# Kernel tuning notes

Measured on AMD Instinct MI355X. Metric: run time of the kernel, lower is better.

Reference implementation:

```python
import jax, jax.numpy as jnp
import numpy as np

B, N, D, H, F, K, L, V, E, C = 8, 256, 768, 8, 3072, 128, 8, 32, 1024, 2
HD = D // H
LN_EPS = 1e-3  # keras LayerNormalization default epsilon
GAUSS_A = (2.0 * 3.14159) ** 0.5  # constant from source


def _ln(x, g, b):
    m = jnp.mean(x, axis=-1, keepdims=True)
    v = jnp.mean((x - m) ** 2, axis=-1, keepdims=True)
    return (x - m) * jax.lax.rsqrt(v + LN_EPS) * g + b


def _gelu(x):
    return jax.nn.gelu(x, approximate=False)  # keras 'gelu' is exact


def setup_inputs() -> dict:
    key = jax.random.key(0)
    ks = iter(jax.random.split(key, 40))
    s = 0.02
    inp = {
        'dist': jax.random.uniform(next(ks), (B, N, N), jnp.float32) * 10.0,
        'tok_emb': jax.random.normal(next(ks), (V, D), jnp.float32) * s,
        'gmeans': jax.random.uniform(next(ks), (K,), jnp.float32) * 3.0,
        'gstds': jax.random.uniform(next(ks), (K,), jnp.float32) * 3.0,
        'gmul': jnp.ones((E, 1), jnp.float32),
        'gbias': jnp.zeros((E, 1), jnp.float32),
        'gp1w': jax.random.normal(next(ks), (K, K), jnp.float32) * s,
        'gp1b': jnp.zeros((K,), jnp.float32),
        'gp2w': jax.random.normal(next(ks), (K, H), jnp.float32) * s,
        'gp2b': jnp.zeros((H,), jnp.float32),
        'emb_ln_g': jnp.ones((D,), jnp.float32),
        'emb_ln_b': jnp.zeros((D,), jnp.float32),
        'Wq': jax.random.normal(next(ks), (L, D, D), jnp.float32) * s,
        'bq': jnp.zeros((L, D), jnp.float32),
        'Wo': jax.random.normal(next(ks), (L, D, D), jnp.float32) * s,
        'bo': jnp.zeros((L, D), jnp.float32),
        'ln1g': jnp.ones((L, D), jnp.float32),
        'ln1b': jnp.zeros((L, D), jnp.float32),
        'W1': jax.random.normal(next(ks), (L, D, F), jnp.float32) * s,
        'b1': jnp.zeros((L, F), jnp.float32),
        'W2': jax.random.normal(next(ks), (L, F, D), jnp.float32) * s,
        'b2': jnp.zeros((L, D), jnp.float32),
        'ln2g': jnp.ones((L, D), jnp.float32),
        'ln2b': jnp.zeros((L, D), jnp.float32),
        'fin_ln_g': jnp.ones((D,), jnp.float32),
        'fin_ln_b': jnp.zeros((D,), jnp.float32),
        'cls_w1': jax.random.normal(next(ks), (D, D), jnp.float32) * s,
        'cls_b1': jnp.zeros((D,), jnp.float32),
        'cls_w2': jax.random.normal(next(ks), (D, C), jnp.float32) * s,
        'cls_b2': jnp.zeros((C,), jnp.float32),
        'tokens': jax.random.randint(next(ks), (B, N), 0, V, jnp.int64),
        'edge_type': jax.random.randint(next(ks), (B, N, N), 0, E, jnp.int64),
    }
    return inp


def _forward(dist, tok_emb, gmeans, gstds, gmul, gbias, gp1w, gp1b, gp2w, gp2b,
             emb_ln_g, emb_ln_b, Wq, bq, Wo, bo, ln1g, ln1b, W1, b1, W2, b2,
             ln2g, ln2b, fin_ln_g, fin_ln_b, cls_w1, cls_b1, cls_w2, cls_b2,
             tokens, edge_type):
    # --- Gaussian pairwise bias ---
    mul = gmul[edge_type][..., 0]      # (B,N,N)
    add = gbias[edge_type][..., 0]     # (B,N,N)
    y = mul * dist + add               # (B,N,N)
    std = jnp.abs(gstds) + 1e-5        # (K,)
    g = jnp.exp(-0.5 * ((y[..., None] - gmeans) / std) ** 2) / (GAUSS_A * std)  # (B,N,N,K)
    pb = _gelu(g @ gp1w + gp1b) @ gp2w + gp2b   # (B,N,N,H)
    attn_bias = jnp.transpose(pb, (0, 3, 1, 2))  # (B,H,N,N)

    # --- encoder (pre-LN), NB: wq is shared for q/k/v as in source ---
    x = tok_emb[tokens]                # (B,N,D)
    x = _ln(x, emb_ln_g, emb_ln_b)
    scale = 1.0 / np.sqrt(HD).astype(np.float32)

    def split_heads(t):
        return t.reshape(B, N, H, HD).transpose(0, 2, 1, 3)  # (B,H,N,HD)

    for i in range(L):
        r = x
        h = _ln(x, ln1g[i], ln1b[i])
        q = split_heads((h @ Wq[i] + bq[i]) * scale)
        k = split_heads(h @ Wq[i] + bq[i])
        v = split_heads(h @ Wq[i] + bq[i])
        s = jnp.einsum('bhnd,bhmd->bhnm', q, k) + attn_bias
        p = jax.nn.softmax(s, axis=-1)
        o = jnp.einsum('bhnm,bhmd->bhnd', p, v)
        o = o.transpose(0, 2, 1, 3).reshape(B, N, D) @ Wo[i] + bo[i]
        x = o + r
        r = x
        h = _ln(x, ln2g[i], ln2b[i])
        x = _gelu(h @ W1[i] + b1[i]) @ W2[i] + b2[i] + r
    x = _ln(x, fin_ln_g, fin_ln_b)

    # --- classification head on CLS token ---
    cls = x[:, 0, :]
    return _gelu(cls @ cls_w1 + cls_b1) @ cls_w2 + cls_b2  # (B,C)


def reference(dist, tok_emb, gmeans, gstds, gmul, gbias, gp1w, gp1b, gp2w, gp2b,
              emb_ln_g, emb_ln_b, Wq, bq, Wo, bo, ln1g, ln1b, W1, b1, W2, b2,
              ln2g, ln2b, fin_ln_g, fin_ln_b, cls_w1, cls_b1, cls_w2, cls_b2,
              tokens, edge_type):
    return _forward(dist, tok_emb, gmeans, gstds, gmul, gbias, gp1w, gp1b, gp2w,
                    gp2b, emb_ln_g, emb_ln_b, Wq, bq, Wo, bo, ln1g, ln1b, W1, b1,
                    W2, b2, ln2g, ln2b, fin_ln_g, fin_ln_b, cls_w1, cls_b1,
                    cls_w2, cls_b2, tokens, edge_type)
```

## Files before the change

### kernel.cpp

```cpp
#include <hip/hip_runtime.h>
#include <hip/hip_bf16.h>
#include <math.h>


#define DEV_INLINE __device__ __forceinline__

typedef __attribute__((ext_vector_type(8))) short short8v;
typedef __attribute__((ext_vector_type(4))) short short4v;
typedef __attribute__((ext_vector_type(4))) float f32x4;

typedef __attribute__((address_space(1))) const unsigned int GLD_SRC;
typedef __attribute__((address_space(3))) unsigned int LDS_DST;

DEV_INLINE void gload16(const unsigned short* g, unsigned short* l) {
  __builtin_amdgcn_global_load_lds((GLD_SRC*)(const void*)g, (LDS_DST*)(void*)l, 16, 0, 0);
}
DEV_INLINE unsigned short f2bf(float f) {
  unsigned u = __float_as_uint(f);
  return (unsigned short)((u + 0x7fffu + ((u >> 16) & 1u)) >> 16);
}
DEV_INLINE unsigned short f2bf_hw(float f) {
  __hip_bfloat16 h = __float2bfloat16(f);
  unsigned short u; __builtin_memcpy(&u, &h, 2); return u;
}
DEV_INLINE float gelu_f(float v) {
  return 0.5f * v * (1.0f + erff(v * 0.70710678118654752f));
}
DEV_INLINE float gelu_tanh(float x) {
  float x2 = x * x;
  float t  = x * fmaf(0.044715f, x2, 1.0f);
  float e  = __builtin_amdgcn_exp2f(2.3022082f * t);
  return x * e * __frcp_rn(e + 1.0f);
}
DEV_INLINE f32x4 zero4() { f32x4 z; z[0]=0.f; z[1]=0.f; z[2]=0.f; z[3]=0.f; return z; }

__global__ __launch_bounds__(256) void k_cast_t(
    const float* __restrict__ W, unsigned short* __restrict__ Wt, int K, int N)
{
  __shared__ float s[64][68];
  const int tid = threadIdx.x;
  const size_t lay = (size_t)blockIdx.z * K * N;
  const int k0 = blockIdx.x * 64, n0 = blockIdx.y * 64;
  const int r = tid >> 4, c4 = (tid & 15) << 2;
  #pragma unroll
  for (int i = 0; i < 4; ++i)
    *(float4*)&s[r + i * 16][c4] =
        *(const float4*)(W + lay + (size_t)(k0 + r + i * 16) * N + n0 + c4);
  __syncthreads();
  const int n = tid & 63, kc = (tid >> 6) << 4;
  short8v v0, v1;
  #pragma unroll
  for (int j = 0; j < 8; ++j) v0[j] = (short)f2bf(s[kc + j][n]);
  #pragma unroll
  for (int j = 0; j < 8; ++j) v1[j] = (short)f2bf(s[kc + 8 + j][n]);
  unsigned short* dst = Wt + lay + (size_t)(n0 + n) * K + k0 + kc;
  *(short8v*)dst = v0;
  *(short8v*)(dst + 8) = v1;
}

template<int BN, int EPI>
__global__ __launch_bounds__(256) void k_gemm(
    const unsigned short* __restrict__ A, const unsigned short* __restrict__ Bt,
    const float* __restrict__ bias,
    void* __restrict__ C0, void* __restrict__ C1, int N, int Kfull, int Klen)
{
  constexpr int NB = BN / 32;
  __shared__ __align__(16) unsigned short As[2][128 * 64];
  __shared__ __align__(16) unsigned short Bs[2][BN * 64];
  const int tid = threadIdx.x;
  const int l = tid & 63;
  const int w = tid >> 6, wr = w >> 1, wc = w & 1;
  const int row0 = blockIdx.x * 128, col0 = blockIdx.y * BN;
  const int z = blockIdx.z;
  const int Koff = z * Klen;
  const int NT = Klen >> 6;

  const int lr = l >> 3;
  const int lc = ((l & 7) ^ lr) << 3;
  const unsigned short* gA[4];
  #pragma unroll
  for (int i = 0; i < 4; ++i)
    gA[i] = A + (size_t)(row0 + w * 32 + i * 8 + lr) * Kfull + Koff + lc;
  const unsigned short* gB[NB];
  #pragma unroll
  for (int i = 0; i < NB; ++i)
    gB[i] = Bt + (size_t)(col0 + w * 8 * NB + i * 8 + lr) * Kfull + Koff + lc;

  #pragma unroll
  for (int i = 0; i < 4; ++i) gload16(gA[i], &As[0][(w * 32 + i * 8) * 64]);
  #pragma unroll
  for (int i = 0; i < NB; ++i) gload16(gB[i], &Bs[0][(w * 8 * NB + i * 8) * 64]);

  f32x4 acc[4][NB];
  #pragma unroll
  for (int mi = 0; mi < 4; ++mi)
    #pragma unroll
    for (int ni = 0; ni < NB; ++ni) acc[mi][ni] = zero4();

  for (int kt = 0; kt < NT; ++kt) {
    const int cur = kt & 1;
    __syncthreads();
    if (kt + 1 < NT) {
      #pragma unroll
      for (int i = 0; i < 4; ++i)
        gload16(gA[i] + (kt + 1) * 64, &As[cur ^ 1][(w * 32 + i * 8) * 64]);
      #pragma unroll
      for (int i = 0; i < NB; ++i)
        gload16(gB[i] + (kt + 1) * 64, &Bs[cur ^ 1][(w * 8 * NB + i * 8) * 64]);
    }
    #pragma unroll
    for (int kk = 0; kk < 2; ++kk) {
      short8v af[4], bf_[NB];
      #pragma unroll
      for (int mi = 0; mi < 4; ++mi) {
        int rw = wr * 64 + mi * 16 + (l & 15);
        int kb = (kk * 64 + ((l >> 4) << 4)) ^ ((rw & 7) << 4);
        af[mi] = *(const short8v*)&As[cur][rw * 64 + (kb >> 1)];
      }
      #pragma unroll
      for (int ni = 0; ni < NB; ++ni) {
        int rw = wc * (BN / 2) + ni * 16 + (l & 15);
        int kb = (kk * 64 + ((l >> 4) << 4)) ^ ((rw & 7) << 4);
        bf_[ni] = *(const short8v*)&Bs[cur][rw * 64 + (kb >> 1)];
      }
      #pragma unroll
      for (int mi = 0; mi < 4; ++mi)
        #pragma unroll
        for (int ni = 0; ni < NB; ++ni)
          acc[mi][ni] = __builtin_amdgcn_mfma_f32_16x16x32_bf16(
              af[mi], bf_[ni], acc[mi][ni], 0, 0, 0);
    }
  }

  const int cl = l & 15, rg = (l >> 4) << 2;
  void* Cv = (EPI == 3 && z) ? C1 : C0;
  float bv[NB];
  #pragma unroll
  for (int ni = 0; ni < NB; ++ni)
    bv[ni] = (EPI == 3 && z) ? 0.f : bias[col0 + wc * (BN / 2) + ni * 16 + cl];
  #pragma unroll
  for (int mi = 0; mi < 4; ++mi) {
    #pragma unroll
    for (int r = 0; r < 4; ++r) {
      size_t rowg = row0 + wr * 64 + mi * 16 + rg + r;
      #pragma unroll
      for (int ni = 0; ni < NB; ++ni) {
        size_t off = rowg * N + col0 + wc * (BN / 2) + ni * 16 + cl;
        float v = acc[mi][ni][r] + bv[ni];
        if (EPI == 0) ((unsigned short*)Cv)[off] = f2bf(v);
        if (EPI == 1) ((unsigned short*)Cv)[off] = f2bf(gelu_f(v));
        if (EPI == 3) ((float*)Cv)[off] = v;
      }
    }
  }
}

__global__ __launch_bounds__(256) void k_gauss(
    const float* __restrict__ dist, const int* __restrict__ edge,
    const float* __restrict__ gmul, const float* __restrict__ gbias,
    const float* __restrict__ gmeans, const float* __restrict__ gstds,
    const unsigned short* __restrict__ gp1wt, const float* __restrict__ gp1b,
    const float* __restrict__ gp2w, const float* __restrict__ gp2b,
    float* __restrict__ bias_out)
{
  __shared__ float4 prm[128];
  __shared__ float b2s[8];
  __shared__ __align__(16) unsigned short w2t[16 * 136];
  __shared__ __align__(16) unsigned short t1[4][2048];
  const int tid = threadIdx.x, l = tid & 63, w = tid >> 6;
  const int pos0 = blockIdx.x * 64;

  if (tid < 128) {
    float sd = fabsf(gstds[tid]) + 1e-5f;
    float inv = 1.0f / sd;
    prm[tid] = make_float4(gmeans[tid], -0.72134752f * inv * inv,
                           0.39894268f * inv, gp1b[tid]);
  }
  if (tid < 8) b2s[tid] = gp2b[tid];
  for (int i = tid; i < 2048; i += 256) {
    int hh = i & 15, k = i >> 4;
    w2t[hh * 136 + k] = (hh < 8) ? f2bf(gp2w[k * 8 + hh]) : (unsigned short)0;
  }
  __syncthreads();

  const int p = pos0 + w * 16 + (l & 15);
  const int et = edge[p];
  const float y = gmul[et] * dist[p] + gbias[et];

  short8v ga[4];
  #pragma unroll
  for (int ks = 0; ks < 4; ++ks) {
    #pragma unroll
    for (int j = 0; j < 8; ++j) {
      int k = ks * 32 + ((l >> 4) << 3) + j;
      float4 pk = prm[k];
      float d = y - pk.x;
      ga[ks][j] = (short)f2bf_hw(__builtin_amdgcn_exp2f(pk.y * d * d) * pk.z);
    }
  }
  f32x4 acc[8];
  #pragma unroll
  for (int n = 0; n < 8; ++n) {
    acc[n] = zero4();
    const unsigned short* bp = gp1wt + (size_t)(n * 16 + (l & 15)) * 128 + ((l >> 4) << 3);
    #pragma unroll
    for (int ks = 0; ks < 4; ++ks)
      acc[n] = __builtin_amdgcn_mfma_f32_16x16x32_bf16(
          ga[ks], *(const short8v*)(bp + ks * 32), acc[n], 0, 0, 0);
  }
  unsigned short* tw = t1[w];
  {
    const int rb = (l >> 4) << 2;
    #pragma unroll
    for (int n = 0; n < 8; ++n) {
      int col2 = (n * 16 + (l & 15)) * 2;
      float bb = prm[n * 16 + (l & 15)].w;
      #pragma unroll
      for (int r = 0; r < 4; ++r) {
        int row = rb + r;
        int swz = ((row & 3) << 4) ^ ((row >> 2) << 5);
        tw[(row * 256 + (col2 ^ swz)) >> 1] = f2bf_hw(gelu_tanh(acc[n][r] + bb));
      }
    }
  }
  f32x4 o4 = zero4();
  {
    const int row = l & 15;
    const int swz = ((row & 3) << 4) ^ ((row >> 2) << 5);
    #pragma unroll
    for (int ks = 0; ks < 4; ++ks) {
      short8v af = *(const short8v*)&tw[(row * 256 + ((ks * 64 + ((l >> 4) << 4)) ^ swz)) >> 1];
      short8v bf_ = *(const short8v*)&w2t[(l & 15) * 136 + ks * 32 + ((l >> 4) << 3)];
      o4 = __builtin_amdgcn_mfma_f32_16x16x32_bf16(af, bf_, o4, 0, 0, 0);
    }
  }
  const int hh = l & 15;
  if (hh < 8) {
    int b = pos0 >> 16;
    int ij = (pos0 & 65535) + w * 16 + ((l >> 4) << 2);
    float4 vv;
    vv.x = o4[0] + b2s[hh]; vv.y = o4[1] + b2s[hh];
    vv.z = o4[2] + b2s[hh]; vv.w = o4[3] + b2s[hh];
    *(float4*)(bias_out + ((size_t)((b << 3) + hh) << 16) + ij) = vv;
  }
}

__global__ __launch_bounds__(256) void k_embed_ln(
    const float* __restrict__ emb, const int* __restrict__ tokens,
    const float* __restrict__ g, const float* __restrict__ bp,
    float* __restrict__ out)
{
  __shared__ float red[4], red2[4];
  const int t = threadIdx.x;
  const int row = blockIdx.x;
  const float* xr = emb + (size_t)tokens[row] * 768;
  float v0 = xr[t], v1 = xr[t + 256], v2 = xr[t + 512];
  float s = v0 + v1 + v2;
  #pragma unroll
  for (int o = 32; o; o >>= 1) s += __shfl_down(s, o);
  if ((t & 63) == 0) red[t >> 6] = s;
  __syncthreads();
  float mean = (red[0] + red[1] + red[2] + red[3]) * (1.0f / 768.0f);
  float d0 = v0 - mean, d1 = v1 - mean, d2 = v2 - mean;
  float q = d0 * d0 + d1 * d1 + d2 * d2;
  #pragma unroll
  for (int o = 32; o; o >>= 1) q += __shfl_down(q, o);
  if ((t & 63) == 0) red2[t >> 6] = q;
  __syncthreads();
  float rstd = rsqrtf((red2[0] + red2[1] + red2[2] + red2[3]) * (1.0f / 768.0f) + 1e-3f);
  float* outr = out + (size_t)row * 768;
  outr[t]       = d0 * rstd * g[t]       + bp[t];
  outr[t + 256] = d1 * rstd * g[t + 256] + bp[t + 256];
  outr[t + 512] = d2 * rstd * g[t + 512] + bp[t + 512];
}

__global__ __launch_bounds__(256) void k_ln_bf(
    const float* __restrict__ in, const float* __restrict__ g,
    const float* __restrict__ bp, unsigned short* __restrict__ out)
{
  __shared__ float red[4], red2[4];
  const int t = threadIdx.x;
  const size_t base = (size_t)blockIdx.x * 768;
  const float* xr = in + base;
  float v0 = xr[t], v1 = xr[t + 256], v2 = xr[t + 512];
  float s = v0 + v1 + v2;
  #pragma unroll
  for (int o = 32; o; o >>= 1) s += __shfl_down(s, o);
  if ((t & 63) == 0) red[t >> 6] = s;
  __syncthreads();
  float mean = (red[0] + red[1] + red[2] + red[3]) * (1.0f / 768.0f);
  float d0 = v0 - mean, d1 = v1 - mean, d2 = v2 - mean;
  float q = d0 * d0 + d1 * d1 + d2 * d2;
  #pragma unroll
  for (int o = 32; o; o >>= 1) q += __shfl_down(q, o);
  if ((t & 63) == 0) red2[t >> 6] = q;
  __syncthreads();
  float rstd = rsqrtf((red2[0] + red2[1] + red2[2] + red2[3]) * (1.0f / 768.0f) + 1e-3f);
  unsigned short* outr = out + base;
  outr[t]       = f2bf(d0 * rstd * g[t]       + bp[t]);
  outr[t + 256] = f2bf(d1 * rstd * g[t + 256] + bp[t + 256]);
  outr[t + 512] = f2bf(d2 * rstd * g[t + 512] + bp[t + 512]);
}

template<int DO_LN>
__global__ __launch_bounds__(256) void k_fuse(
    const float* __restrict__ p0, const float* __restrict__ p1,
    const float* __restrict__ g, const float* __restrict__ bp,
    float* __restrict__ x, unsigned short* __restrict__ h)
{
  __shared__ float red[4], red2[4];
  const int t = threadIdx.x;
  const size_t base = (size_t)blockIdx.x * 768;
  float v0 = p0[base + t]       + p1[base + t]       + x[base + t];
  float v1 = p0[base + t + 256] + p1[base + t + 256] + x[base + t + 256];
  float v2 = p0[base + t + 512] + p1[base + t + 512] + x[base + t + 512];
  x[base + t]       = v0;
  x[base + t + 256] = v1;
  x[base + t + 512] = v2;
  if (DO_LN) {
    float s = v0 + v1 + v2;
    #pragma unroll
    for (int o = 32; o; o >>= 1) s += __shfl_down(s, o);
    if ((t & 63) == 0) red[t >> 6] = s;
    __syncthreads();
    float mean = (red[0] + red[1] + red[2] + red[3]) * (1.0f / 768.0f);
    float d0 = v0 - mean, d1 = v1 - mean, d2 = v2 - mean;
    float q = d0 * d0 + d1 * d1 + d2 * d2;
    #pragma unroll
    for (int o = 32; o; o >>= 1) q += __shfl_down(q, o);
    if ((t & 63) == 0) red2[t >> 6] = q;
    __syncthreads();
    float rstd = rsqrtf((red2[0] + red2[1] + red2[2] + red2[3]) * (1.0f / 768.0f) + 1e-3f);
    h[base + t]       = f2bf(d0 * rstd * g[t]       + bp[t]);
    h[base + t + 256] = f2bf(d1 * rstd * g[t + 256] + bp[t + 256]);
    h[base + t + 512] = f2bf(d2 * rstd * g[t + 512] + bp[t + 512]);
  }
}

__global__ __launch_bounds__(256) void k_transV(
    const unsigned short* __restrict__ P, unsigned short* __restrict__ Vt)
{
  __shared__ unsigned short s[64 * 100];
  const int tid = threadIdx.x;
  const int i0 = blockIdx.x * 64, bh = blockIdx.y, b = bh >> 3, h = bh & 7;
  const unsigned short* Pb = P + ((size_t)b * 256 + i0) * 768 + h * 96;
  #pragma unroll
  for (int i = 0; i < 6; ++i) {
    int o = (tid + i * 256) * 8;
    int row = o / 192, c = o - row * 192;
    *(short4v*)&s[row * 100 + (c >> 1)] =
        *(const short4v*)(Pb + (size_t)row * 768 + (c >> 1));
  }
  __syncthreads();
  #pragma unroll
  for (int i = 0; i < 3; ++i) {
    int u = tid + i * 256;
    int d = u >> 3, tk = (u & 7) << 3;
    short8v v;
    #pragma unroll
    for (int j = 0; j < 8; ++j) v[j] = (short)s[(tk + j) * 100 + d];
    *(short8v*)(Vt + ((size_t)bh * 96 + d) * 256 + i0 + tk) = v;
  }
}

__global__ __launch_bounds__(256) void k_attn(
    const unsigned short* __restrict__ P, const unsigned short* __restrict__ Vt,
    const float* __restrict__ bias, unsigned short* __restrict__ O)
{
  __shared__ __align__(16) unsigned short pl[4][4096];
  const int tid = threadIdx.x, l = tid & 63, w = tid >> 6;
  const int i0 = blockIdx.x << 6, bh = blockIdx.y, b = bh >> 3, hh = bh & 7;
  const unsigned short* Pb = P + (size_t)b * 196608 + hh * 96;

  short8v aq[3];
  const int rq = i0 + w * 16 + (l & 15);
  #pragma unroll
  for (int ks = 0; ks < 3; ++ks)
    aq[ks] = *(const short8v*)(Pb + (size_t)rq * 768 + ks * 32 + ((l >> 4) << 3));

  f32x4 acc[16];
  #pragma unroll
  for (int n = 0; n < 16; ++n) {
    acc[n] = zero4();
    const unsigned short* kp = Pb + (size_t)(n * 16 + (l & 15)) * 768 + ((l >> 4) << 3);
    #pragma unroll
    for (int ks = 0; ks < 3; ++ks)
      acc[n] = __builtin_amdgcn_mfma_f32_16x16x32_bf16(
          aq[ks], *(const short8v*)(kp + ks * 32), acc[n], 0, 0, 0);
  }

  const float scale = 0.10206207261596577f;
  float inv[4];
  unsigned short* plw = pl[w];
  const size_t brow = ((size_t)bh * 256 + i0 + w * 16 + ((l >> 4) << 2)) * 256 + (l & 15);
  #pragma unroll
  for (int r = 0; r < 4; ++r) {
    const float* bptr = bias + brow + (size_t)r * 256;
    float m = -1e30f;
    #pragma unroll
    for (int n = 0; n < 16; ++n) {
      float v = acc[n][r] * scale + bptr[n * 16];
      acc[n][r] = v;
      m = fmaxf(m, v);
    }
    m = fmaxf(m, __shfl_xor(m, 1)); m = fmaxf(m, __shfl_xor(m, 2));
    m = fmaxf(m, __shfl_xor(m, 4)); m = fmaxf(m, __shfl_xor(m, 8));
    const int rowL = ((l >> 4) << 2) + r;
    const int swz = ((rowL & 3) << 4) ^ ((rowL >> 2) << 5);
    const int cb = (l & 15) << 1;
    float s = 0.f;
    #pragma unroll
    for (int n = 0; n < 16; ++n) {
      float e = __expf(acc[n][r] - m);
      s += e;
      plw[(rowL * 512 + ((cb + (n << 5)) ^ swz)) >> 1] = f2bf_hw(e);
    }
    s += __shfl_xor(s, 1); s += __shfl_xor(s, 2);
    s += __shfl_xor(s, 4); s += __shfl_xor(s, 8);
    inv[r] = 1.0f / s;
  }

  const int rowA = l & 15;
  const int swzA = ((rowA & 3) << 4) ^ ((rowA >> 2) << 5);
  short8v pa[8];
  #pragma unroll
  for (int ks = 0; ks < 8; ++ks)
    pa[ks] = *(const short8v*)&plw[(rowA * 512 + ((ks * 64 + ((l >> 4) << 4)) ^ swzA)) >> 1];

  unsigned short* Ob = O + ((size_t)b * 256 + i0 + w * 16 + ((l >> 4) << 2)) * 768
                       + hh * 96 + (l & 15);
  #pragma unroll
  for (int n = 0; n < 6; ++n) {
    f32x4 a2 = zero4();
    const unsigned short* vb = Vt + ((size_t)bh * 96 + n * 16 + (l & 15)) * 256 + ((l >> 4) << 3);
    #pragma unroll
    for (int ks = 0; ks < 8; ++ks)
      a2 = __builtin_amdgcn_mfma_f32_16x16x32_bf16(
          pa[ks], *(const short8v*)(vb + ks * 32), a2, 0, 0, 0);
    #pragma unroll
    for (int r = 0; r < 4; ++r)
      Ob[(size_t)r * 768 + n * 16] = f2bf(a2[r] * inv[r]);
  }
}

__global__ __launch_bounds__(256) void k_cls(
    const float* __restrict__ x, const float* __restrict__ fg,
    const float* __restrict__ fb, const float* __restrict__ w1,
    const float* __restrict__ b1, const float* __restrict__ w2,
    const float* __restrict__ b2, float* __restrict__ out)
{
  __shared__ float ln[768];
  __shared__ float t1[768];
  __shared__ float red[8];
  __shared__ float r2[8];
  const int t = threadIdx.x;
  const int b = blockIdx.x;
  const float* xr = x + (size_t)b * 256 * 768;
  float v0 = xr[t], v1 = xr[t + 256], v2 = xr[t + 512];
  float s = v0 + v1 + v2;
  #pragma unroll
  for (int o = 32; o; o >>= 1) s += __shfl_down(s, o);
  if ((t & 63) == 0) red[t >> 6] = s;
  __syncthreads();
  float mean = (red[0] + red[1] + red[2] + red[3]) * (1.0f / 768.0f);
  float d0 = v0 - mean, d1 = v1 - mean, d2 = v2 - mean;
  float q = d0 * d0 + d1 * d1 + d2 * d2;
  #pragma unroll
  for (int o = 32; o; o >>= 1) q += __shfl_down(q, o);
  if ((t & 63) == 0) red[4 + (t >> 6)] = q;
  __syncthreads();
  float rstd = rsqrtf((red[4] + red[5] + red[6] + red[7]) * (1.0f / 768.0f) + 1e-3f);
  ln[t]       = d0 * rstd * fg[t]       + fb[t];
  ln[t + 256] = d1 * rstd * fg[t + 256] + fb[t + 256];
  ln[t + 512] = d2 * rstd * fg[t + 512] + fb[t + 512];
  __syncthreads();
  float a0 = b1[t], a1 = b1[t + 256], a2 = b1[t + 512];
  for (int d = 0; d < 768; ++d) {
    float lv = ln[d];
    a0 = fmaf(lv, w1[d * 768 + t], a0);
    a1 = fmaf(lv, w1[d * 768 + t + 256], a1);
    a2 = fmaf(lv, w1[d * 768 + t + 512], a2);
  }
  t1[t]       = gelu_f(a0);
  t1[t + 256] = gelu_f(a1);
  t1[t + 512] = gelu_f(a2);
  __syncthreads();
  float p0 = 0.f, p1 = 0.f;
  #pragma unroll
  for (int oo = 0; oo < 3; ++oo) {
    int d = t + oo * 256;
    p0 = fmaf(t1[d], w2[d * 2], p0);
    p1 = fmaf(t1[d], w2[d * 2 + 1], p1);
  }
  #pragma unroll
  for (int o = 32; o; o >>= 1) {
    p0 += __shfl_down(p0, o);
    p1 += __shfl_down(p1, o);
  }
  if ((t & 63) == 0) { r2[t >> 6] = p0; r2[4 + (t >> 6)] = p1; }
  __syncthreads();
  if (t == 0) {
    out[b * 2]     = r2[0] + r2[1] + r2[2] + r2[3] + b2[0];
    out[b * 2 + 1] = r2[4] + r2[5] + r2[6] + r2[7] + b2[1];
  }
}

extern "C" void kernel_launch(void* const* d_in, const int* in_sizes, int n_in,
                              void* d_out, int out_size, void* d_ws, size_t ws_size,
                              hipStream_t stream)
{
  const float* dist    = (const float*)d_in[0];
  const float* tok_emb = (const float*)d_in[1];
  const float* gmeans  = (const float*)d_in[2];
  const float* gstds   = (const float*)d_in[3];
  const float* gmul    = (const float*)d_in[4];
  const float* gbias   = (const float*)d_in[5];
  const float* gp1w    = (const float*)d_in[6];
  const float* gp1b    = (const float*)d_in[7];
  const float* gp2w    = (const float*)d_in[8];
  const float* gp2b    = (const float*)d_in[9];
  const float* embg    = (const float*)d_in[10];
  const float* embb    = (const float*)d_in[11];
  const float* Wq      = (const float*)d_in[12];
  const float* bq      = (const float*)d_in[13];
  const float* Wo      = (const float*)d_in[14];
  const float* bo      = (const float*)d_in[15];
  const float* ln1g    = (const float*)d_in[16];
  const float* ln1b    = (const float*)d_in[17];
  const float* W1      = (const float*)d_in[18];
  const float* b1      = (const float*)d_in[19];
  const float* W2      = (const float*)d_in[20];
  const float* b2      = (const float*)d_in[21];
  const float* ln2g    = (const float*)d_in[22];
  const float* ln2b    = (const float*)d_in[23];
  const float* fing    = (const float*)d_in[24];
  const float* finb    = (const float*)d_in[25];
  const float* cw1     = (const float*)d_in[26];
  const float* cb1     = (const float*)d_in[27];
  const float* cw2     = (const float*)d_in[28];
  const float* cb2     = (const float*)d_in[29];
  const int*   tokens  = (const int*)d_in[30];
  const int*   edge    = (const int*)d_in[31];

  float* ws   = (float*)d_ws;
  float* bias = ws;
  float* x    = bias + 4194304;
  float* p0   = x + 1572864;
  float* p1   = p0 + 1572864;
  unsigned short* hO  = (unsigned short*)(p1 + 1572864);
  unsigned short* P   = hO + 1572864;
  unsigned short* Vt  = P + 1572864;
  unsigned short* f1  = Vt + 1572864;
  unsigned short* Wqt = f1 + 6291456;
  unsigned short* Wot = Wqt + 4718592;
  unsigned short* W1t = Wot + 4718592;
  unsigned short* W2t = W1t + 18874368;
  unsigned short* g1t = W2t + 18874368;

  k_cast_t<<<dim3(12, 12, 8), 256, 0, stream>>>(Wq, Wqt, 768, 768);
  k_cast_t<<<dim3(12, 12, 8), 256, 0, stream>>>(Wo, Wot, 768, 768);
  k_cast_t<<<dim3(12, 48, 8), 256, 0, stream>>>(W1, W1t, 768, 3072);
  k_cast_t<<<dim3(48, 12, 8), 256, 0, stream>>>(W2, W2t, 3072, 768);
  k_cast_t<<<dim3(2, 2, 1), 256, 0, stream>>>(gp1w, g1t, 128, 128);

  k_gauss<<<8192, 256, 0, stream>>>(dist, edge, gmul, gbias, gmeans, gstds,
                                    g1t, gp1b, gp2w, gp2b, bias);
  k_embed_ln<<<2048, 256, 0, stream>>>(tok_emb, tokens, embg, embb, x);
  k_ln_bf<<<2048, 256, 0, stream>>>(x, ln1g, ln1b, hO);

  for (int l = 0; l < 8; ++l) {
    k_gemm<64, 0><<<dim3(16, 12, 1), 256, 0, stream>>>(
        hO, Wqt + (size_t)l * 589824, bq + l * 768, P, nullptr, 768, 768, 768);
    k_transV<<<dim3(4, 64), 256, 0, stream>>>(P, Vt);
    k_attn<<<dim3(4, 64), 256, 0, stream>>>(P, Vt, bias, hO);
    k_gemm<64, 3><<<dim3(16, 12, 2), 256, 0, stream>>>(
        hO, Wot + (size_t)l * 589824, bo + l * 768, p0, p1, 768, 768, 384);
    k_fuse<1><<<2048, 256, 0, stream>>>(p0, p1, ln2g + l * 768, ln2b + l * 768, x, hO);
    k_gemm<128, 1><<<dim3(16, 24, 1), 256, 0, stream>>>(
        hO, W1t + (size_t)l * 2359296, b1 + l * 3072, f1, nullptr, 3072, 768, 768);
    k_gemm<64, 3><<<dim3(16, 12, 2), 256, 0, stream>>>(
        f1, W2t + (size_t)l * 2359296, b2 + l * 768, p0, p1, 768, 3072, 1536);
    if (l < 7)
      k_fuse<1><<<2048, 256, 0, stream>>>(p0, p1, ln1g + (l + 1) * 768,
                                          ln1b + (l + 1) * 768, x, hO);
    else
      k_fuse<0><<<2048, 256, 0, stream>>>(p0, p1, nullptr, nullptr, x, hO);
  }
  k_cls<<<8, 256, 0, stream>>>(x, fing, finb, cw1, cb1, cw2, cb2, (float*)d_out);
}
```

Measured before the change: 1.238 ms.

## Split-K Q projection, fuse V transpose, halve attention blocks, fold gauss coef

The Q projection now runs as a split-K GEMM into two fp32 partials, and a new combine kernel sums them, writes the bf16 P and scatters the transposed V in one pass, replacing the separate transpose kernel. Attention blocks shrink to 32 query rows with 2 waves each, doubling the grid. The Gaussian normalisation coefficient is folded into the bf16 gp1 weights, and the embedding LayerNorm is fused with the first layer LayerNorm. The changes aim at more parallelism and fewer launches, but the V scatter writes are uncoalesced and the split-K adds fp32 partial traffic.

```diff
diff --git a/kernel.cpp b/kernel.cpp
--- a/kernel.cpp
+++ b/kernel.cpp
@@ -29,7 +29,8 @@
 DEV_INLINE float gelu_tanh(float x) {
   float x2 = x * x;
   float t  = x * fmaf(0.044715f, x2, 1.0f);
-  float e  = __builtin_amdgcn_exp2f(2.3022082f * t);
+  float a  = fminf(2.3022082f * t, 252.0f);
+  float e  = __builtin_amdgcn_exp2f(a);
   return x * e * __frcp_rn(e + 1.0f);
 }
 DEV_INLINE f32x4 zero4() { f32x4 z; z[0]=0.f; z[1]=0.f; z[2]=0.f; z[3]=0.f; return z; }
@@ -56,6 +57,17 @@
   unsigned short* dst = Wt + lay + (size_t)(n0 + n) * K + k0 + kc;
   *(short8v*)dst = v0;
   *(short8v*)(dst + 8) = v1;
+}
+
+__global__ __launch_bounds__(128) void k_cast_g1(
+    const float* __restrict__ gp1w, const float* __restrict__ gstds,
+    unsigned short* __restrict__ g1t)
+{
+  const int k = threadIdx.x;
+  const int n = blockIdx.x;
+  float sd = fabsf(gstds[k]) + 1e-5f;
+  float coef = 0.39894268f / sd;
+  g1t[n * 128 + k] = f2bf(coef * gp1w[k * 128 + n]);
 }
 
 template<int BN, int EPI>
@@ -163,7 +175,7 @@
     const float* __restrict__ gp2w, const float* __restrict__ gp2b,
     float* __restrict__ bias_out)
 {
-  __shared__ float4 prm[128];
+  __shared__ float mean_s[128], c2_s[128], b1s[128];
   __shared__ float b2s[8];
   __shared__ __align__(16) unsigned short w2t[16 * 136];
   __shared__ __align__(16) unsigned short t1[4][2048];
@@ -173,8 +185,9 @@
   if (tid < 128) {
     float sd = fabsf(gstds[tid]) + 1e-5f;
     float inv = 1.0f / sd;
-    prm[tid] = make_float4(gmeans[tid], -0.72134752f * inv * inv,
-                           0.39894268f * inv, gp1b[tid]);
+    mean_s[tid] = gmeans[tid];
+    c2_s[tid] = -0.72134752f * inv * inv;
+    b1s[tid] = gp1b[tid];
   }
   if (tid < 8) b2s[tid] = gp2b[tid];
   for (int i = tid; i < 2048; i += 256) {
@@ -193,9 +206,8 @@
     #pragma unroll
     for (int j = 0; j < 8; ++j) {
       int k = ks * 32 + ((l >> 4) << 3) + j;
-      float4 pk = prm[k];
-      float d = y - pk.x;
-      ga[ks][j] = (short)f2bf_hw(__builtin_amdgcn_exp2f(pk.y * d * d) * pk.z);
+      float d = y - mean_s[k];
+      ga[ks][j] = (short)f2bf_hw(__builtin_amdgcn_exp2f(c2_s[k] * d * d));
     }
   }
   f32x4 acc[8];
@@ -214,7 +226,7 @@
     #pragma unroll
     for (int n = 0; n < 8; ++n) {
       int col2 = (n * 16 + (l & 15)) * 2;
-      float bb = prm[n * 16 + (l & 15)].w;
+      float bb = b1s[n * 16 + (l & 15)];
       #pragma unroll
       for (int r = 0; r < 4; ++r) {
         int row = rb + r;
@@ -245,10 +257,11 @@
   }
 }
 
-__global__ __launch_bounds__(256) void k_embed_ln(
+__global__ __launch_bounds__(256) void k_embed2(
     const float* __restrict__ emb, const int* __restrict__ tokens,
-    const float* __restrict__ g, const float* __restrict__ bp,
-    float* __restrict__ out)
+    const float* __restrict__ eg, const float* __restrict__ eb,
+    const float* __restrict__ g1, const float* __restrict__ bp1,
+    float* __restrict__ x, unsigned short* __restrict__ h)
 {
   __shared__ float red[4], red2[4];
   const int t = threadIdx.x;
@@ -268,38 +281,48 @@
   if ((t & 63) == 0) red2[t >> 6] = q;
   __syncthreads();
   float rstd = rsqrtf((red2[0] + red2[1] + red2[2] + red2[3]) * (1.0f / 768.0f) + 1e-3f);
-  float* outr = out + (size_t)row * 768;
-  outr[t]       = d0 * rstd * g[t]       + bp[t];
-  outr[t + 256] = d1 * rstd * g[t + 256] + bp[t + 256];
-  outr[t + 512] = d2 * rstd * g[t + 512] + bp[t + 512];
-}
-
-__global__ __launch_bounds__(256) void k_ln_bf(
-    const float* __restrict__ in, const float* __restrict__ g,
-    const float* __restrict__ bp, unsigned short* __restrict__ out)
-{
-  __shared__ float red[4], red2[4];
-  const int t = threadIdx.x;
-  const size_t base = (size_t)blockIdx.x * 768;
-  const float* xr = in + base;
-  float v0 = xr[t], v1 = xr[t + 256], v2 = xr[t + 512];
-  float s = v0 + v1 + v2;
+  float* outr = x + (size_t)row * 768;
+  float y0 = d0 * rstd * eg[t]       + eb[t];
+  float y1 = d1 * rstd * eg[t + 256] + eb[t + 256];
+  float y2 = d2 * rstd * eg[t + 512] + eb[t + 512];
+  outr[t] = y0; outr[t + 256] = y1; outr[t + 512] = y2;
+  __syncthreads();
+  s = y0 + y1 + y2;
   #pragma unroll
   for (int o = 32; o; o >>= 1) s += __shfl_down(s, o);
   if ((t & 63) == 0) red[t >> 6] = s;
   __syncthreads();
-  float mean = (red[0] + red[1] + red[2] + red[3]) * (1.0f / 768.0f);
-  float d0 = v0 - mean, d1 = v1 - mean, d2 = v2 - mean;
-  float q = d0 * d0 + d1 * d1 + d2 * d2;
+  mean = (red[0] + red[1] + red[2] + red[3]) * (1.0f / 768.0f);
+  d0 = y0 - mean; d1 = y1 - mean; d2 = y2 - mean;
+  q = d0 * d0 + d1 * d1 + d2 * d2;
   #pragma unroll
   for (int o = 32; o; o >>= 1) q += __shfl_down(q, o);
   if ((t & 63) == 0) red2[t >> 6] = q;
   __syncthreads();
-  float rstd = rsqrtf((red2[0] + red2[1] + red2[2] + red2[3]) * (1.0f / 768.0f) + 1e-3f);
-  unsigned short* outr = out + base;
-  outr[t]       = f2bf(d0 * rstd * g[t]       + bp[t]);
-  outr[t + 256] = f2bf(d1 * rstd * g[t + 256] + bp[t + 256]);
-  outr[t + 512] = f2bf(d2 * rstd * g[t + 512] + bp[t + 512]);
+  rstd = rsqrtf((red2[0] + red2[1] + red2[2] + red2[3]) * (1.0f / 768.0f) + 1e-3f);
+  unsigned short* hr = h + (size_t)row * 768;
+  hr[t]       = f2bf(d0 * rstd * g1[t]       + bp1[t]);
+  hr[t + 256] = f2bf(d1 * rstd * g1[t + 256] + bp1[t + 256]);
+  hr[t + 512] = f2bf(d2 * rstd * g1[t + 512] + bp1[t + 512]);
+}
+
+__global__ __launch_bounds__(256) void k_combP(
+    const float* __restrict__ p0, const float* __restrict__ p1,
+    unsigned short* __restrict__ P, unsigned short* __restrict__ Vt)
+{
+  const int t = threadIdx.x;
+  const int row = blockIdx.x;
+  const int b = row >> 8, tok = row & 255;
+  const size_t base = (size_t)row * 768;
+  #pragma unroll
+  for (int i = 0; i < 3; ++i) {
+    int c = t + i * 256;
+    float v = p0[base + c] + p1[base + c];
+    unsigned short bv = f2bf(v);
+    P[base + c] = bv;
+    int h = c / 96, d = c - h * 96;
+    Vt[((size_t)((b << 3) + h) * 96 + d) * 256 + tok] = bv;
+  }
 }
 
 template<int DO_LN>
@@ -337,39 +360,13 @@
   }
 }
 
-__global__ __launch_bounds__(256) void k_transV(
-    const unsigned short* __restrict__ P, unsigned short* __restrict__ Vt)
-{
-  __shared__ unsigned short s[64 * 100];
-  const int tid = threadIdx.x;
-  const int i0 = blockIdx.x * 64, bh = blockIdx.y, b = bh >> 3, h = bh & 7;
-  const unsigned short* Pb = P + ((size_t)b * 256 + i0) * 768 + h * 96;
-  #pragma unroll
-  for (int i = 0; i < 6; ++i) {
-    int o = (tid + i * 256) * 8;
-    int row = o / 192, c = o - row * 192;
-    *(short4v*)&s[row * 100 + (c >> 1)] =
-        *(const short4v*)(Pb + (size_t)row * 768 + (c >> 1));
-  }
-  __syncthreads();
-  #pragma unroll
-  for (int i = 0; i < 3; ++i) {
-    int u = tid + i * 256;
-    int d = u >> 3, tk = (u & 7) << 3;
-    short8v v;
-    #pragma unroll
-    for (int j = 0; j < 8; ++j) v[j] = (short)s[(tk + j) * 100 + d];
-    *(short8v*)(Vt + ((size_t)bh * 96 + d) * 256 + i0 + tk) = v;
-  }
-}
-
-__global__ __launch_bounds__(256) void k_attn(
+__global__ __launch_bounds__(128) void k_attn(
     const unsigned short* __restrict__ P, const unsigned short* __restrict__ Vt,
     const float* __restrict__ bias, unsigned short* __restrict__ O)
 {
-  __shared__ __align__(16) unsigned short pl[4][4096];
+  __shared__ __align__(16) unsigned short pl[2][4096];
   const int tid = threadIdx.x, l = tid & 63, w = tid >> 6;
-  const int i0 = blockIdx.x << 6, bh = blockIdx.y, b = bh >> 3, hh = bh & 7;
+  const int i0 = blockIdx.x << 5, bh = blockIdx.y, b = bh >> 3, hh = bh & 7;
   const unsigned short* Pb = P + (size_t)b * 196608 + hh * 96;
 
   short8v aq[3];
@@ -557,22 +554,20 @@
   unsigned short* W2t = W1t + 18874368;
   unsigned short* g1t = W2t + 18874368;
 
+  k_cast_g1<<<128, 128, 0, stream>>>(gp1w, gstds, g1t);
+  k_gauss<<<8192, 256, 0, stream>>>(dist, edge, gmul, gbias, gmeans, gstds,
+                                    g1t, gp1b, gp2w, gp2b, bias);
   k_cast_t<<<dim3(12, 12, 8), 256, 0, stream>>>(Wq, Wqt, 768, 768);
   k_cast_t<<<dim3(12, 12, 8), 256, 0, stream>>>(Wo, Wot, 768, 768);
   k_cast_t<<<dim3(12, 48, 8), 256, 0, stream>>>(W1, W1t, 768, 3072);
   k_cast_t<<<dim3(48, 12, 8), 256, 0, stream>>>(W2, W2t, 3072, 768);
-  k_cast_t<<<dim3(2, 2, 1), 256, 0, stream>>>(gp1w, g1t, 128, 128);
-
-  k_gauss<<<8192, 256, 0, stream>>>(dist, edge, gmul, gbias, gmeans, gstds,
-                                    g1t, gp1b, gp2w, gp2b, bias);
-  k_embed_ln<<<2048, 256, 0, stream>>>(tok_emb, tokens, embg, embb, x);
-  k_ln_bf<<<2048, 256, 0, stream>>>(x, ln1g, ln1b, hO);
+  k_embed2<<<2048, 256, 0, stream>>>(tok_emb, tokens, embg, embb, ln1g, ln1b, x, hO);
 
   for (int l = 0; l < 8; ++l) {
-    k_gemm<64, 0><<<dim3(16, 12, 1), 256, 0, stream>>>(
-        hO, Wqt + (size_t)l * 589824, bq + l * 768, P, nullptr, 768, 768, 768);
-    k_transV<<<dim3(4, 64), 256, 0, stream>>>(P, Vt);
-    k_attn<<<dim3(4, 64), 256, 0, stream>>>(P, Vt, bias, hO);
+    k_gemm<64, 3><<<dim3(16, 12, 2), 256, 0, stream>>>(
+        hO, Wqt + (size_t)l * 589824, bq + l * 768, p0, p1, 768, 768, 384);
+    k_combP<<<2048, 256, 0, stream>>>(p0, p1, P, Vt);
+    k_attn<<<dim3(8, 64), 128, 0, stream>>>(P, Vt, bias, hO);
     k_gemm<64, 3><<<dim3(16, 12, 2), 256, 0, stream>>>(
         hO, Wot + (size_t)l * 589824, bo + l * 768, p0, p1, 768, 768, 384);
     k_fuse<1><<<2048, 256, 0, stream>>>(p0, p1, ln2g + l * 768, ln2b + l * 768, x, hO);
```

After: 1.314 ms. 6.2% more time.
